# Performance work log

Hardware: AMD Instinct MI355X
Metric: run time of the kernel (lower is better)

## Reference

```python
import jax, jax.numpy as jnp
import numpy as np

DIM = 192; HEADS = 6; WS = 8; OVERLAP = 2; PAD = 3; STRIDE = WS - OVERLAP; HID = DIM * 4

_coords = np.stack(np.meshgrid(np.arange(WS), np.arange(WS), indexing='ij'), 0).reshape(2, -1)
_rel = (_coords[:, :, None] - _coords[:, None, :]).transpose(1, 2, 0).astype(np.int64)
_rel[..., 0] += WS - 1; _rel[..., 1] += WS - 1; _rel[..., 0] *= 2 * WS - 1
REL_IDX = jnp.asarray(_rel.sum(-1).reshape(-1))  # (WS^2 * WS^2,)


def _ln_c(x, g, b):
    # LayerNorm over channel dim of NCHW (LayerNormProxy)
    mu = jnp.mean(x, axis=1, keepdims=True)
    var = jnp.mean((x - mu) ** 2, axis=1, keepdims=True)
    return (x - mu) * jax.lax.rsqrt(var + 1e-5) * g[:, None, None] + b[:, None, None]


def _conv1x1(x, w, b):
    return jnp.einsum('bchw,oc->bohw', x, w) + b[:, None, None]


def _dwconv3(x, w, b):
    y = jax.lax.conv_general_dilated(x, w, (1, 1), ((1, 1), (1, 1)),
                                     feature_group_count=x.shape[1],
                                     dimension_numbers=('NCHW', 'OIHW', 'NCHW'))
    return y + b[:, None, None]


def _unfold(x, k, s, p):
    # F.unfold: (B,C,H,W) -> (B, C*k*k, L) with (C,kh,kw) channel order, row-major windows
    B, C, H, W = x.shape
    xp = jnp.pad(x, ((0, 0), (0, 0), (p, p), (p, p)))
    Lh = (H + 2 * p - k) // s + 1; Lw = (W + 2 * p - k) // s + 1
    ih = (jnp.arange(Lh) * s)[:, None] + jnp.arange(k)  # (Lh,k)
    iw = (jnp.arange(Lw) * s)[:, None] + jnp.arange(k)  # (Lw,k)
    t = xp[:, :, ih, :][:, :, :, :, iw]                 # (B,C,Lh,k,Lw,k)
    t = t.transpose(0, 1, 3, 5, 2, 4)                   # (B,C,k,k,Lh,Lw)
    return t.reshape(B, C * k * k, Lh * Lw)


def _fold(cols, h, w, k, s, p):
    # F.fold: (B, C*k*k, L) -> (B,C,h,w), summing overlaps
    B = cols.shape[0]
    Lh = (h + 2 * p - k) // s + 1; Lw = (w + 2 * p - k) // s + 1
    C = cols.shape[1] // (k * k)
    t = cols.reshape(B, C, k, k, Lh, Lw).transpose(0, 1, 4, 2, 5, 3)  # (B,C,Lh,k,Lw,k)
    ih = (jnp.arange(Lh) * s)[:, None] + jnp.arange(k)
    iw = (jnp.arange(Lw) * s)[:, None] + jnp.arange(k)
    out = jnp.zeros((B, C, h + 2 * p, w + 2 * p), cols.dtype)
    out = out.at[:, :, ih[:, :, None, None], iw[None, None, :, :]].add(t)
    return out[:, :, p:p + h, p:p + w]


def _reverse(win, h, w):
    B, L, nH, ws2, ch = win.shape
    cols = win.transpose(0, 2, 4, 3, 1).reshape(B, nH * ch * ws2, L)
    return _fold(cols, h, w, WS, STRIDE, PAD)


def _hft(x, w, b):
    # HFTAttention: high-frequency residual of multi-scale avg pools, dw-conv sigmoid gate
    B, C, h, ww = x.shape
    a = 3.0 * x
    for s in (2, 4, 8):
        pool = x.reshape(B, C, h // s, s, ww // s, s).mean(axis=(3, 5))
        a = a - jnp.repeat(jnp.repeat(pool, s, axis=2), s, axis=3)
    return jax.nn.sigmoid(_dwconv3(a, w, b)) * x


def _forward(x, n1g, n1b, qkv_w, qkv_b, temp, rpb, proj_w, proj_b, hft_w, hft_b,
             n2g, n2b, fc1_w, fc1_b, sgn_g, sgn_b, sg_w, sg_b, fc2_w, fc2_b):
    B, C, H, W = x.shape
    ch = C // HEADS
    y = _conv1x1(_ln_c(x, n1g, n1b), qkv_w, qkv_b)       # (B,3C,H,W)
    cols = _unfold(y, WS, STRIDE, PAD)
    L = cols.shape[-1]
    win = cols.reshape(B, 3 * HEADS, ch, WS * WS, L).transpose(0, 4, 1, 3, 2)  # (B,L,3H,ws2,ch)
    q = win[:, :, :HEADS] * temp[None, None]
    k = win[:, :, HEADS:2 * HEADS]
    v = win[:, :, 2 * HEADS:]
    attn = jnp.einsum('blhic,blhjc->blhij', q, k)
    bias = rpb[REL_IDX].reshape(WS * WS, WS * WS, HEADS).transpose(2, 0, 1)
    attn = attn + bias[None, None]
    e = jnp.exp(attn - jnp.max(attn, axis=-1, keepdims=True))
    s = jnp.sum(e, axis=-1, keepdims=True)               # (B,L,H,ws2,1)
    s_img = _reverse(s, H, W)                            # (B,HEADS,H,W): folded softmax denom
    o = jnp.einsum('blhij,blhjc->blhic', e, v)
    o_img = _reverse(o, H, W).reshape(B, HEADS, ch, H, W)
    out = (o_img / s_img[:, :, None]).reshape(B, C, H, W)
    out = _hft(_conv1x1(out, proj_w, proj_b), hft_w, hft_b)
    x1 = x + out
    z = jax.nn.gelu(_conv1x1(_ln_c(x1, n2g, n2b), fc1_w, fc1_b), approximate=False)
    z1, z2 = jnp.split(z, 2, axis=1)
    z = z1 * _dwconv3(_ln_c(z2, sgn_g, sgn_b), sg_w, sg_b)
    return x1 + _conv1x1(z, fc2_w, fc2_b)


def setup_inputs() -> dict:
    key = jax.random.key(0)
    ks = jax.random.split(key, 8)
    B, Hi, Wi = 4, 128, 128
    f = jnp.float32
    return {
        'x': jax.random.normal(ks[0], (B, DIM, Hi, Wi), f),
        'n1g': jnp.ones((DIM,), f), 'n1b': jnp.zeros((DIM,), f),
        'qkv_w': jax.random.normal(ks[1], (3 * DIM, DIM), f) * 0.02,
        'qkv_b': jnp.zeros((3 * DIM,), f),
        'temp': jnp.ones((HEADS, 1, 1), f),
        'rpb': jax.random.normal(ks[2], ((2 * WS - 1) ** 2, HEADS), f) * 0.02,
        'proj_w': jax.random.normal(ks[3], (DIM, DIM), f) * 0.02,
        'proj_b': jnp.zeros((DIM,), f),
        'hft_w': jax.random.normal(ks[4], (DIM, 1, 3, 3), f) * 0.02,
        'hft_b': jnp.zeros((DIM,), f),
        'n2g': jnp.ones((DIM,), f), 'n2b': jnp.zeros((DIM,), f),
        'fc1_w': jax.random.normal(ks[5], (HID, DIM), f) * 0.02,
        'fc1_b': jnp.zeros((HID,), f),
        'sgn_g': jnp.ones((HID // 2,), f), 'sgn_b': jnp.zeros((HID // 2,), f),
        'sg_w': jax.random.normal(ks[6], (HID // 2, 1, 3, 3), f) * 0.02,
        'sg_b': jnp.zeros((HID // 2,), f),
        'fc2_w': jax.random.normal(ks[7], (DIM, HID // 2), f) * 0.02,
        'fc2_b': jnp.zeros((DIM,), f),
    }


def reference(x, n1g, n1b, qkv_w, qkv_b, temp, rpb, proj_w, proj_b, hft_w, hft_b,
              n2g, n2b, fc1_w, fc1_b, sgn_g, sgn_b, sg_w, sg_b, fc2_w, fc2_b):
    return _forward(x, n1g, n1b, qkv_w, qkv_b, temp, rpb, proj_w, proj_b, hft_w, hft_b,
                    n2g, n2b, fc1_w, fc1_b, sgn_g, sgn_b, sg_w, sg_b, fc2_w, fc2_b)
```

## Files before the change

### kernel.cpp

```cpp
#include <hip/hip_runtime.h>
#include <math.h>

static constexpr int B_    = 4;
static constexpr int C_    = 192;
static constexpr int NPIX  = 16384;
static constexpr int PTOT  = B_ * NPIX;
static constexpr int HEADS = 6;
static constexpr int STR   = 6;
static constexpr int LH    = 22;
static constexpr int LWIN  = LH * LH;
static constexpr int NWIN  = B_ * LWIN;

typedef short bf16x8 __attribute__((ext_vector_type(8)));
typedef float f32x4  __attribute__((ext_vector_type(4)));

__device__ __forceinline__ unsigned short f2bf(float f) {
    union { float f; unsigned int u; } v; v.f = f;
    return (unsigned short)((v.u + 0x8000u) >> 16);
}
__device__ __forceinline__ float bf2f(unsigned short h) {
    union { unsigned int u; float f; } v; v.u = ((unsigned int)h) << 16;
    return v.f;
}
__device__ __forceinline__ unsigned int pack2bf(float a, float b) {
    union { float f; unsigned int u; } x, y; x.f = a; y.f = b;
    return __builtin_amdgcn_perm(y.u + 0x8000u, x.u + 0x8000u, 0x07060302u);
}
__device__ __forceinline__ float gelu_f(float v) {
    float vv = v * v;
    float u  = v * fmaf(vv, 0.0713548162f, 1.5957691216f);
    float ue = (u > 80.f) ? 80.f : u;
    float e  = __expf(ue);
    float r  = __builtin_amdgcn_rcpf(e + 1.f);
    return v * e * r;
}

__global__ __launch_bounds__(256) void prep_k(const float* __restrict__ W, const float* __restrict__ g,
                                              const float* __restrict__ bln, const float* __restrict__ bias,
                                              int M, int K,
                                              unsigned short* __restrict__ wgb, float* __restrict__ wsum,
                                              float* __restrict__ wb) {
    int o = blockIdx.x * 256 + threadIdx.x;
    if (o >= M) return;
    float sum = 0.f, bb = 0.f;
    for (int c = 0; c < K; ++c) {
        float wv = W[(size_t)o * K + c];
        float wgv = wv * g[c];
        wgb[(size_t)o * K + c] = f2bf(wgv);
        sum += wgv;
        bb += wv * bln[c];
    }
    wsum[o] = sum;
    wb[o] = bb + bias[o];
}

__global__ __launch_bounds__(256) void wcvt_k(const float* __restrict__ W, unsigned short* __restrict__ Wb, int n) {
    int i = blockIdx.x * 256 + threadIdx.x;
    if (i < n) Wb[i] = f2bf(W[i]);
}

template <typename T, bool LNS>
__global__ __launch_bounds__(256) void transpose_k(const T* __restrict__ in, unsigned short* __restrict__ out,
                                                   int Cn, int bstride, float2* __restrict__ ps) {
    __shared__ float tile[64][65];
    int n0 = blockIdx.x << 6, c0 = blockIdx.y << 6, b = blockIdx.z;
    int t = threadIdx.x, r = t >> 2, cg = (t & 3) << 4;
    const T* ib = in + (size_t)b * bstride;
    if constexpr (sizeof(T) == 4) {
        const float4* src = (const float4*)(ib + (size_t)(c0 + r) * NPIX + n0 + cg);
        #pragma unroll
        for (int j = 0; j < 4; ++j) {
            float4 v = src[j];
            tile[r][cg + 4 * j + 0] = v.x; tile[r][cg + 4 * j + 1] = v.y;
            tile[r][cg + 4 * j + 2] = v.z; tile[r][cg + 4 * j + 3] = v.w;
        }
    } else {
        const uint4* src = (const uint4*)((const unsigned short*)ib + (size_t)(c0 + r) * NPIX + n0 + cg);
        uint4 v0 = src[0], v1 = src[1];
        unsigned int arr[8] = {v0.x, v0.y, v0.z, v0.w, v1.x, v1.y, v1.z, v1.w};
        #pragma unroll
        for (int j = 0; j < 8; ++j) {
            tile[r][cg + 2 * j]     = bf2f((unsigned short)(arr[j] & 0xFFFFu));
            tile[r][cg + 2 * j + 1] = bf2f((unsigned short)(arr[j] >> 16));
        }
    }
    __syncthreads();
    unsigned int pk[8];
    float s = 0.f, s2 = 0.f;
    #pragma unroll
    for (int j = 0; j < 8; ++j) {
        float a  = tile[cg + 2 * j][r];
        float c2 = tile[cg + 2 * j + 1][r];
        if (LNS) { s += a + c2; s2 += a * a + c2 * c2; }
        pk[j] = pack2bf(a, c2);
    }
    uint4* dst = (uint4*)(out + ((size_t)(b << 14) + n0 + r) * Cn + c0 + cg);
    dst[0] = make_uint4(pk[0], pk[1], pk[2], pk[3]);
    dst[1] = make_uint4(pk[4], pk[5], pk[6], pk[7]);
    if (LNS) {
        s  += __shfl_xor(s, 1);  s  += __shfl_xor(s, 2);
        s2 += __shfl_xor(s2, 1); s2 += __shfl_xor(s2, 2);
        if ((t & 3) == 0)
            ps[((b * gridDim.y + blockIdx.y) << 14) + n0 + r] = make_float2(s, s2);
    }
}

__global__ __launch_bounds__(256) void lnfin_k(const float2* __restrict__ ps, int nch, float invC,
                                               float* __restrict__ mu, float* __restrict__ rs) {
    int p = blockIdx.x * 256 + threadIdx.x;
    int b = p >> 14, n = p & (NPIX - 1);
    float s = 0.f, s2 = 0.f;
    for (int c = 0; c < nch; ++c) {
        float2 v = ps[((b * nch + c) << 14) + n];
        s += v.x; s2 += v.y;
    }
    float m = s * invC;
    mu[p] = m;
    rs[p] = rsqrtf(s2 * invC - m * m + 1e-5f);
}

__global__ __launch_bounds__(256) void lnstats_z2_k(const unsigned short* __restrict__ z,
                                                    float* __restrict__ mu, float* __restrict__ rs) {
    __shared__ float red[2][4][64];
    int n0 = blockIdx.x << 6, b = blockIdx.y;
    int t = threadIdx.x;
    int px = n0 + (t & 63), cg = t >> 6;
    float s = 0.f, s2 = 0.f;
    for (int c = cg; c < 384; c += 4) {
        float v = bf2f(z[((size_t)(b * 768 + 384 + c) << 14) + px]);
        s += v; s2 += v * v;
    }
    red[0][cg][t & 63] = s;
    red[1][cg][t & 63] = s2;
    __syncthreads();
    if (t < 64) {
        float ss  = red[0][0][t] + red[0][1][t] + red[0][2][t] + red[0][3][t];
        float ss2 = red[1][0][t] + red[1][1][t] + red[1][2][t] + red[1][3][t];
        float m = ss * (1.f / 384.f);
        mu[(b << 14) + n0 + t] = m;
        rs[(b << 14) + n0 + t] = rsqrtf(ss2 * (1.f / 384.f) - m * m + 1e-5f);
    }
}

template <int KK, int MPB, int ACT, bool LN, bool RES, bool OBF>
__global__ __launch_bounds__(256) void gemm2_k(const unsigned short* __restrict__ Wb,
                                               const unsigned short* __restrict__ Xt,
                                               void* __restrict__ outv,
                                               const float* __restrict__ mu, const float* __restrict__ rs,
                                               const float* __restrict__ wsum, const float* __restrict__ wb,
                                               const float* __restrict__ resid, int M) {
    constexpr int LDK    = KK + 8;
    constexpr int KSTEPS = KK / 32;
    constexpr int PFG    = (KSTEPS > 6) ? 6 : KSTEPS;
    __shared__ unsigned short xs[64 * LDK];

    int t = threadIdx.x;
    int pt = blockIdx.x;
    int b  = pt >> 8;
    int n0 = (pt & 255) << 6;

    const unsigned short* xg = Xt + (size_t)(b * NPIX + n0) * KK;
    constexpr int NJ = KK / 8;
    #pragma unroll
    for (int i = 0; i < 64 * NJ / 256; ++i) {
        int c = i * 256 + t;
        int p, j;
        if (KK == 192) { p = (c * 2731) >> 16; j = c - p * 24; }
        else           { int q = c >> 4; p = (q * 21846) >> 16; j = c - p * 48; }
        uint4 v = *(const uint4*)(xg + (size_t)c * 8);
        *(uint4*)&xs[p * LDK + j * 8] = v;
    }
    __syncthreads();

    int w  = t >> 6, l = t & 63;
    int wr = w >> 1, wc = w & 1;
    int lr = l & 15, kb = l >> 4;
    int pw = wr * 32;

    bf16x8 afr[KSTEPS][2];
    #pragma unroll
    for (int ks = 0; ks < KSTEPS; ++ks)
        #pragma unroll
        for (int m = 0; m < 2; ++m)
            afr[ks][m] = *(const bf16x8*)&xs[(pw + m * 16 + lr) * LDK + ks * 32 + kb * 8];

    float rsv[2][4], murs[2][4];
    if (LN) {
        #pragma unroll
        for (int m = 0; m < 2; ++m) {
            int nidx = n0 + pw + m * 16 + kb * 4;
            #pragma unroll
            for (int r = 0; r < 4; ++r) {
                float mv = mu[(b << 14) + nidx + r];
                rsv[m][r] = rs[(b << 14) + nidx + r];
                murs[m][r] = mv * rsv[m][r];
            }
        }
    }

    int ocbase = blockIdx.y * MPB;
    #pragma unroll
    for (int oc = 0; oc < MPB; ++oc) {
        int ow = ((ocbase + oc) << 6) + wc * 32;
        f32x4 acc[2][2];
        #pragma unroll
        for (int m = 0; m < 2; ++m)
            #pragma unroll
            for (int n = 0; n < 2; ++n) acc[m][n] = (f32x4){0.f, 0.f, 0.f, 0.f};

        #pragma unroll
        for (int kg = 0; kg < KSTEPS; kg += PFG) {
            bf16x8 bfr[PFG][2];
            #pragma unroll
            for (int kk = 0; kk < PFG; ++kk)
                #pragma unroll
                for (int n = 0; n < 2; ++n)
                    bfr[kk][n] = *(const bf16x8*)(Wb + (size_t)(ow + n * 16 + lr) * KK + (kg + kk) * 32 + kb * 8);
            #pragma unroll
            for (int kk = 0; kk < PFG; ++kk)
                #pragma unroll
                for (int m = 0; m < 2; ++m)
                    #pragma unroll
                    for (int n = 0; n < 2; ++n)
                        acc[m][n] = __builtin_amdgcn_mfma_f32_16x16x32_bf16(afr[kg + kk][m], bfr[kk][n], acc[m][n], 0, 0, 0);
        }

        #pragma unroll
        for (int m = 0; m < 2; ++m) {
            int nidx = n0 + pw + m * 16 + kb * 4;
            #pragma unroll
            for (int n = 0; n < 2; ++n) {
                int o = ow + n * 16 + lr;
                float wbv = wb[o];
                float wsv = 0.f; if (LN) wsv = wsum[o];
                size_t obase = (((size_t)b * M + o) << 14) + nidx;
                float rv[4] = {0.f, 0.f, 0.f, 0.f};
                if (RES) {
                    float4 rr = *(const float4*)(resid + obase);
                    rv[0] = rr.x; rv[1] = rr.y; rv[2] = rr.z; rv[3] = rr.w;
                }
                float vo[4];
                #pragma unroll
                for (int r = 0; r < 4; ++r) {
                    float a = acc[m][n][r];
                    float v;
                    if (LN) { float t1 = fmaf(-murs[m][r], wsv, wbv); v = fmaf(rsv[m][r], a, t1); }
                    else    v = a + wbv;
                    if (ACT == 1) v = gelu_f(v);
                    vo[r] = v + rv[r];
                }
                if (OBF) {
                    uint2 u;
                    u.x = pack2bf(vo[0], vo[1]);
                    u.y = pack2bf(vo[2], vo[3]);
                    *(uint2*)((unsigned short*)outv + obase) = u;
                } else {
                    float4 f = {vo[0], vo[1], vo[2], vo[3]};
                    *(float4*)((float*)outv + obase) = f;
                }
            }
        }
    }
}

__global__ __launch_bounds__(64) void attn_mfma_k(const unsigned short* __restrict__ qkv,
                                                  const float* __restrict__ rpb,
                                                  const float* __restrict__ temp,
                                                  unsigned short* __restrict__ o_win,
                                                  float* __restrict__ s_win) {
    __shared__ unsigned short p_lds[64 * 72];
    __shared__ float rp[225];
    int wh = blockIdx.x;
    int head = wh % HEADS;
    int bw = wh / HEADS;
    int b = bw / LWIN, l = bw % LWIN;
    int sh = l / LH, sw = l % LH;
    int h0 = sh * STR - 3, w0 = sw * STR - 3;
    int t = threadIdx.x;
    int lr = t & 15, kb = t >> 4;

    for (int i = t; i < 225; i += 64) rp[i] = rpb[i * HEADS + head];
    float tmp = temp[head];

    const size_t qbase = ((size_t)(b * 576 + head * 32)) << 14;
    const unsigned short* qp = qkv + qbase;
    const unsigned short* kp = qkv + qbase + ((size_t)192 << 14);
    const unsigned short* vp = qkv + qbase + ((size_t)384 << 14);

    bf16x8 kf[4], qf[4];
    #pragma unroll
    for (int m = 0; m < 4; ++m) {
        int jp = m * 16 + lr;
        int hh = h0 + (jp >> 3), ww = w0 + (jp & 7);
        bool ok = ((unsigned)hh < 128u) && ((unsigned)ww < 128u);
        int pix = (hh << 7) + ww;
        #pragma unroll
        for (int j = 0; j < 8; ++j) {
            unsigned short kv = 0, qv = 0;
            if (ok) {
                size_t off = ((size_t)(kb * 8 + j) << 14) + pix;
                kv = kp[off];
                qv = qp[off];
            }
            kf[m][j] = (short)kv;
            qf[m][j] = (short)qv;
        }
    }

    f32x4 st[4][4];
    #pragma unroll
    for (int m = 0; m < 4; ++m)
        #pragma unroll
        for (int n = 0; n < 4; ++n) st[m][n] = (f32x4){0.f, 0.f, 0.f, 0.f};
    #pragma unroll
    for (int m = 0; m < 4; ++m)
        #pragma unroll
        for (int n = 0; n < 4; ++n)
            st[m][n] = __builtin_amdgcn_mfma_f32_16x16x32_bf16(kf[m], qf[n], st[m][n], 0, 0, 0);

    bf16x8 vf[2][2];
    #pragma unroll
    for (int np = 0; np < 2; ++np) {
        #pragma unroll
        for (int ks = 0; ks < 2; ++ks) {
            int hh = h0 + ks * 4 + kb;
            bool okr = (unsigned)hh < 128u;
            const unsigned short* vrow = vp + (((size_t)(np * 16 + lr)) << 14) + (hh << 7) + w0;
            #pragma unroll
            for (int j = 0; j < 8; ++j) {
                int ww = w0 + j;
                unsigned short vv = 0;
                if (okr && (unsigned)ww < 128u) vv = vrow[j];
                vf[np][ks][j] = (short)vv;
            }
        }
    }

    __syncthreads();

    #pragma unroll
    for (int n = 0; n < 4; ++n) {
        int i = n * 16 + lr;
        int iyy = i >> 3, ixx = i & 7;
        #pragma unroll
        for (int m = 0; m < 4; ++m) {
            #pragma unroll
            for (int r = 0; r < 4; ++r) {
                int j = m * 16 + kb * 4 + r;
                int dy = iyy - (j >> 3) + 7;
                int dx = ixx - (j & 7) + 7;
                st[m][n][r] = st[m][n][r] * tmp + rp[dy * 15 + dx];
            }
        }
    }

    #pragma unroll
    for (int n = 0; n < 4; ++n) {
        float mx = -1e30f;
        #pragma unroll
        for (int m = 0; m < 4; ++m)
            #pragma unroll
            for (int r = 0; r < 4; ++r) mx = fmaxf(mx, st[m][n][r]);
        mx = fmaxf(mx, __shfl_xor(mx, 16));
        mx = fmaxf(mx, __shfl_xor(mx, 32));
        float s = 0.f;
        #pragma unroll
        for (int m = 0; m < 4; ++m) {
            #pragma unroll
            for (int r = 0; r < 4; ++r) {
                float e = __expf(st[m][n][r] - mx);
                st[m][n][r] = e;
                s += e;
            }
        }
        s += __shfl_xor(s, 16);
        s += __shfl_xor(s, 32);
        int i = n * 16 + lr;
        if (kb == 0) s_win[(size_t)wh * 64 + i] = s;
        #pragma unroll
        for (int m = 0; m < 4; ++m) {
            *(unsigned int*)&p_lds[i * 72 + m * 16 + kb * 4]     = pack2bf(st[m][n][0], st[m][n][1]);
            *(unsigned int*)&p_lds[i * 72 + m * 16 + kb * 4 + 2] = pack2bf(st[m][n][2], st[m][n][3]);
        }
    }

    __syncthreads();

    f32x4 oc[4][2];
    #pragma unroll
    for (int m = 0; m < 4; ++m)
        #pragma unroll
        for (int np = 0; np < 2; ++np) oc[m][np] = (f32x4){0.f, 0.f, 0.f, 0.f};
    #pragma unroll
    for (int ks = 0; ks < 2; ++ks) {
        bf16x8 pa[4];
        #pragma unroll
        for (int m = 0; m < 4; ++m)
            pa[m] = *(const bf16x8*)&p_lds[(m * 16 + lr) * 72 + ks * 32 + kb * 8];
        #pragma unroll
        for (int m = 0; m < 4; ++m)
            #pragma unroll
            for (int np = 0; np < 2; ++np)
                oc[m][np] = __builtin_amdgcn_mfma_f32_16x16x32_bf16(pa[m], vf[np][ks], oc[m][np], 0, 0, 0);
    }

    unsigned short* ob = o_win + (size_t)wh * 2048;
    #pragma unroll
    for (int m = 0; m < 4; ++m) {
        int ibase = m * 16 + kb * 4;
        #pragma unroll
        for (int np = 0; np < 2; ++np) {
            int c = np * 16 + lr;
            #pragma unroll
            for (int r = 0; r < 4; ++r)
                ob[(ibase + r) * 32 + c] = f2bf(oc[m][np][r]);
        }
    }
}

__device__ __forceinline__ void win_range(int h, int& s0, int& s1) {
    s0 = (h + 1) / 6; if (s0 < 0) s0 = 0;
    s1 = (h + 3) / 6; if (s1 > 21) s1 = 21;
}

__global__ __launch_bounds__(256) void simg_k(const float* __restrict__ s_win, float* __restrict__ s_img) {
    int tid = blockIdx.x * 256 + threadIdx.x;
    if (tid >= B_ * HEADS * NPIX) return;
    int n = tid & (NPIX - 1);
    int bh = tid >> 14;
    int hd = bh % HEADS, b = bh / HEADS;
    int hy = n >> 7, wx = n & 127;
    int sy0, sy1, sx0, sx1;
    win_range(hy, sy0, sy1);
    win_range(wx, sx0, sx1);
    float acc = 0.f;
    for (int sy = sy0; sy <= sy1; ++sy)
        for (int sx = sx0; sx <= sx1; ++sx) {
            int idx = (hy - (sy * 6 - 3)) * 8 + (wx - (sx * 6 - 3));
            acc += s_win[(size_t)((b * LWIN + sy * LH + sx) * HEADS + hd) * 64 + idx];
        }
    s_img[tid] = acc;
}

__global__ __launch_bounds__(256) void fold_k(const unsigned short* __restrict__ o_win,
                                              const float* __restrict__ s_img,
                                              unsigned short* __restrict__ attn_t) {
    int tid = blockIdx.x * 256 + threadIdx.x;
    int q = (int)((((unsigned long long)(tid >> 3)) * 174763ull) >> 19);
    int oct = tid - q * 24;
    int n = q & (NPIX - 1), b = q >> 14;
    int hd = oct >> 2, c8 = (oct & 3) << 3;
    int hy = n >> 7, wx = n & 127;
    int sy0, sy1, sx0, sx1;
    win_range(hy, sy0, sy1);
    win_range(wx, sx0, sx1);
    float acc[8] = {0.f, 0.f, 0.f, 0.f, 0.f, 0.f, 0.f, 0.f};
    for (int sy = sy0; sy <= sy1; ++sy)
        for (int sx = sx0; sx <= sx1; ++sx) {
            int idx = (hy - (sy * 6 - 3)) * 8 + (wx - (sx * 6 - 3));
            const unsigned short* p = o_win + ((size_t)((b * LWIN + sy * LH + sx) * HEADS + hd) * 2048 + idx * 32 + c8);
            uint4 v = *(const uint4*)p;
            unsigned int arr[4] = {v.x, v.y, v.z, v.w};
            #pragma unroll
            for (int j = 0; j < 4; ++j) {
                acc[2 * j]     += bf2f((unsigned short)(arr[j] & 0xFFFFu));
                acc[2 * j + 1] += bf2f((unsigned short)(arr[j] >> 16));
            }
        }
    float inv = __builtin_amdgcn_rcpf(s_img[((b * HEADS + hd) << 14) + n]);
    unsigned int pk[4];
    #pragma unroll
    for (int j = 0; j < 4; ++j)
        pk[j] = pack2bf(acc[2 * j] * inv, acc[2 * j + 1] * inv);
    *(uint4*)&attn_t[((size_t)((b << 14) + n)) * 192 + hd * 32 + c8] = make_uint4(pk[0], pk[1], pk[2], pk[3]);
}

template <typename TI>
__global__ __launch_bounds__(256) void halve_k(const TI* __restrict__ in, float* __restrict__ out, int Win) {
    int Wo = Win >> 1;
    int tot = B_ * C_ * Wo * Wo;
    int tid = blockIdx.x * 256 + threadIdx.x;
    if (tid >= tot) return;
    int xy = tid % (Wo * Wo);
    int bc = tid / (Wo * Wo);
    int y = xy / Wo, x = xy % Wo;
    const TI* p = in + (size_t)bc * Win * Win + (size_t)(2 * y) * Win + 2 * x;
    float a, bq, c, d;
    if constexpr (sizeof(TI) == 2) {
        a = bf2f(p[0]); bq = bf2f(p[1]); c = bf2f(p[Win]); d = bf2f(p[Win + 1]);
    } else {
        a = p[0]; bq = p[1]; c = p[Win]; d = p[Win + 1];
    }
    out[tid] = 0.25f * (a + bq + c + d);
}

__global__ __launch_bounds__(256) void hft_fused_k(const unsigned short* __restrict__ po, const float* __restrict__ x,
                                                   const float* __restrict__ p2, const float* __restrict__ p4,
                                                   const float* __restrict__ p8, const float* __restrict__ hw,
                                                   const float* __restrict__ hb, float* __restrict__ x1) {
    __shared__ float tile[34 * 133];
    int rt = blockIdx.x, ch = blockIdx.y, b = blockIdx.z;
    int bc = b * C_ + ch;
    int y0 = rt << 5;
    int t = threadIdx.x;
    const unsigned short* pob = po + ((size_t)bc << 14);
    const float* p2b = p2 + ((size_t)bc << 12);
    const float* p4b = p4 + ((size_t)bc << 10);
    const float* p8b = p8 + ((size_t)bc << 8);

    for (int idx = t; idx < 34 * 133; idx += 256) {
        int row = idx / 133, col = idx - row * 133;
        int yy = y0 + row - 1, xw = col - 1;
        float val = 0.f;
        if (col < 130 && (unsigned)yy < 128u && (unsigned)xw < 128u) {
            int nn = (yy << 7) + xw;
            val = 3.f * bf2f(pob[nn])
                - p2b[((yy >> 1) << 6) + (xw >> 1)]
                - p4b[((yy >> 2) << 5) + (xw >> 2)]
                - p8b[((yy >> 3) << 4) + (xw >> 3)];
        }
        tile[idx] = val;
    }
    __syncthreads();

    float wv[9];
    #pragma unroll
    for (int k = 0; k < 9; ++k) wv[k] = hw[ch * 9 + k];
    float hbv = hb[ch];

    int r = t & 31, c0 = (t >> 5) << 4;
    int nbase = ((y0 + r) << 7) + c0;
    const float* xb = x + ((size_t)bc << 14);
    float* x1b = x1 + ((size_t)bc << 14);

    float pov[16], xv[16];
    {
        const uint4* pp4 = (const uint4*)(pob + nbase);
        uint4 a0 = pp4[0], a1 = pp4[1];
        unsigned int arr[8] = {a0.x, a0.y, a0.z, a0.w, a1.x, a1.y, a1.z, a1.w};
        #pragma unroll
        for (int j = 0; j < 8; ++j) {
            pov[2 * j]     = bf2f((unsigned short)(arr[j] & 0xFFFFu));
            pov[2 * j + 1] = bf2f((unsigned short)(arr[j] >> 16));
        }
        #pragma unroll
        for (int j4 = 0; j4 < 4; ++j4) {
            float4 xx = *(const float4*)(xb + nbase + 4 * j4);
            xv[4*j4] = xx.x; xv[4*j4+1] = xx.y; xv[4*j4+2] = xx.z; xv[4*j4+3] = xx.w;
        }
    }
    float res[16];
    #pragma unroll
    for (int j = 0; j < 16; ++j) {
        float acc = hbv;
        #pragma unroll
        for (int dy = 0; dy < 3; ++dy)
            #pragma unroll
            for (int dx = 0; dx < 3; ++dx)
                acc += wv[dy * 3 + dx] * tile[(r + dy) * 133 + c0 + j + dx];
        float sg = __builtin_amdgcn_rcpf(1.f + __expf(-acc));
        res[j] = xv[j] + sg * pov[j];
    }
    #pragma unroll
    for (int j4 = 0; j4 < 4; ++j4) {
        float4 o = {res[4*j4], res[4*j4+1], res[4*j4+2], res[4*j4+3]};
        *(float4*)(x1b + nbase + 4 * j4) = o;
    }
}

__global__ __launch_bounds__(256) void sgmul_k(unsigned short* __restrict__ z,
                                               const float* __restrict__ mu3, const float* __restrict__ rs3,
                                               const float* __restrict__ sgn_g, const float* __restrict__ sgn_b,
                                               const float* __restrict__ sg_w, const float* __restrict__ sg_b) {
    __shared__ float tile[34 * 133];
    int rt = blockIdx.x, ch = blockIdx.y, b = blockIdx.z;
    int y0 = rt << 5;
    int t = threadIdx.x;
    const unsigned short* zb = z + ((size_t)(b * 768 + 384 + ch) << 14);
    unsigned short* z1p = z + ((size_t)(b * 768 + ch) << 14);
    const float* mub = mu3 + (b << 14);
    const float* rsb = rs3 + (b << 14);
    float g = sgn_g[ch], bb = sgn_b[ch];

    for (int idx = t; idx < 34 * 133; idx += 256) {
        int row = idx / 133, col = idx - row * 133;
        int yy = y0 + row - 1, xw = col - 1;
        float val = 0.f;
        if (col < 130 && (unsigned)yy < 128u && (unsigned)xw < 128u) {
            int nn = (yy << 7) + xw;
            val = (bf2f(zb[nn]) - mub[nn]) * rsb[nn] * g + bb;
        }
        tile[idx] = val;
    }
    __syncthreads();

    float wv[9];
    #pragma unroll
    for (int k = 0; k < 9; ++k) wv[k] = sg_w[ch * 9 + k];
    float sb = sg_b[ch];

    int r = t & 31, c0 = (t >> 5) << 4;
    int nbase = ((y0 + r) << 7) + c0;

    float res[16];
    #pragma unroll
    for (int j = 0; j < 16; ++j) {
        float acc = sb;
        #pragma unroll
        for (int dy = 0; dy < 3; ++dy)
            #pragma unroll
            for (int dx = 0; dx < 3; ++dx)
                acc += wv[dy * 3 + dx] * tile[(r + dy) * 133 + c0 + j + dx];
        res[j] = acc;
    }
    uint4* zp = (uint4*)(z1p + nbase);
    uint4 v0 = zp[0], v1 = zp[1];
    unsigned int arr[8] = {v0.x, v0.y, v0.z, v0.w, v1.x, v1.y, v1.z, v1.w};
    #pragma unroll
    for (int j = 0; j < 8; ++j) {
        float lo = bf2f((unsigned short)(arr[j] & 0xFFFFu)) * res[2 * j];
        float hi = bf2f((unsigned short)(arr[j] >> 16)) * res[2 * j + 1];
        arr[j] = pack2bf(lo, hi);
    }
    zp[0] = make_uint4(arr[0], arr[1], arr[2], arr[3]);
    zp[1] = make_uint4(arr[4], arr[5], arr[6], arr[7]);
}

extern "C" void kernel_launch(void* const* d_in, const int* in_sizes, int n_in,
                              void* d_out, int out_size, void* d_ws, size_t ws_size,
                              hipStream_t stream) {
    const float* x     = (const float*)d_in[0];
    const float* n1g   = (const float*)d_in[1];
    const float* n1b   = (const float*)d_in[2];
    const float* qkv_w = (const float*)d_in[3];
    const float* qkv_b = (const float*)d_in[4];
    const float* temp  = (const float*)d_in[5];
    const float* rpb   = (const float*)d_in[6];
    const float* proj_w= (const float*)d_in[7];
    const float* proj_b= (const float*)d_in[8];
    const float* hft_w = (const float*)d_in[9];
    const float* hft_b = (const float*)d_in[10];
    const float* n2g   = (const float*)d_in[11];
    const float* n2b   = (const float*)d_in[12];
    const float* fc1_w = (const float*)d_in[13];
    const float* fc1_b = (const float*)d_in[14];
    const float* sgn_g = (const float*)d_in[15];
    const float* sgn_b = (const float*)d_in[16];
    const float* sg_w  = (const float*)d_in[17];
    const float* sg_b  = (const float*)d_in[18];
    const float* fc2_w = (const float*)d_in[19];
    const float* fc2_b = (const float*)d_in[20];
    float* out = (float*)d_out;
    float* w = (float*)d_ws;

    float* mu1 = w;            float* rs1 = w + 65536;
    float* mu2 = w + 131072;   float* rs2 = w + 196608;
    float* mu3 = w + 262144;   float* rs3 = w + 327680;
    unsigned short* wgb_qkv = (unsigned short*)(w + 393216);
    float* wsum_qkv = w + 448512;  float* wb_qkv = w + 449088;
    unsigned short* wgb_fc1 = (unsigned short*)(w + 449664);
    float* wsum_fc1 = w + 523392;  float* wb_fc1 = w + 524160;
    unsigned short* pwb  = (unsigned short*)(w + 524928);
    unsigned short* f2wb = (unsigned short*)(w + 543360);
    unsigned short* xt     = (unsigned short*)(w + 580224);
    unsigned short* attn_t = xt;
    unsigned short* qkvb = (unsigned short*)(w + 6871680);
    unsigned short* proj_out = (unsigned short*)(w + 6871680);
    float* p2 = w + 19454592;  float* p4 = w + 22600320;  float* p8 = w + 23386752;
    unsigned short* x1t  = (unsigned short*)(w + 6871680);
    unsigned short* z1t  = (unsigned short*)(w + 6871680);
    unsigned short* o_win = (unsigned short*)(w + 25746048);
    float* s_win = w + 49535616;
    float* s_img = w + 50279040;
    unsigned short* z = (unsigned short*)(w + 25746048);
    float* x1 = w + 50911872;
    float2* ps = (float2*)(w + 19454592);

    transpose_k<float, true><<<dim3(256, 3, B_), 256, 0, stream>>>(x, xt, 192, 192 * NPIX, ps);
    lnfin_k<<<256, 256, 0, stream>>>(ps, 3, 1.f / 192.f, mu1, rs1);
    prep_k<<<3, 256, 0, stream>>>(qkv_w, n1g, n1b, qkv_b, 576, 192, wgb_qkv, wsum_qkv, wb_qkv);
    gemm2_k<192, 3, 0, true, false, true><<<dim3(1024, 3), 256, 0, stream>>>(
        wgb_qkv, xt, qkvb, mu1, rs1, wsum_qkv, wb_qkv, nullptr, 576);
    attn_mfma_k<<<NWIN * HEADS, 64, 0, stream>>>(qkvb, rpb, temp, o_win, s_win);
    simg_k<<<1536, 256, 0, stream>>>(s_win, s_img);
    fold_k<<<6144, 256, 0, stream>>>(o_win, s_img, attn_t);
    wcvt_k<<<144, 256, 0, stream>>>(proj_w, pwb, 192 * 192);
    gemm2_k<192, 1, 0, false, false, true><<<dim3(1024, 3), 256, 0, stream>>>(
        pwb, attn_t, proj_out, nullptr, nullptr, nullptr, proj_b, nullptr, 192);
    halve_k<unsigned short><<<12288, 256, 0, stream>>>(proj_out, p2, 128);
    halve_k<float><<<3072, 256, 0, stream>>>(p2, p4, 64);
    halve_k<float><<<768, 256, 0, stream>>>(p4, p8, 32);
    hft_fused_k<<<dim3(4, 192, B_), 256, 0, stream>>>(proj_out, x, p2, p4, p8, hft_w, hft_b, x1);
    transpose_k<float, true><<<dim3(256, 3, B_), 256, 0, stream>>>(x1, x1t, 192, 192 * NPIX, ps);
    lnfin_k<<<256, 256, 0, stream>>>(ps, 3, 1.f / 192.f, mu2, rs2);
    prep_k<<<3, 256, 0, stream>>>(fc1_w, n2g, n2b, fc1_b, 768, 192, wgb_fc1, wsum_fc1, wb_fc1);
    gemm2_k<192, 6, 1, true, false, true><<<dim3(1024, 2), 256, 0, stream>>>(
        wgb_fc1, x1t, z, mu2, rs2, wsum_fc1, wb_fc1, nullptr, 768);
    lnstats_z2_k<<<dim3(256, B_), 256, 0, stream>>>(z, mu3, rs3);
    sgmul_k<<<dim3(4, 384, B_), 256, 0, stream>>>(z, mu3, rs3, sgn_g, sgn_b, sg_w, sg_b);
    transpose_k<unsigned short, false><<<dim3(256, 6, B_), 256, 0, stream>>>(z, z1t, 384, 768 * NPIX, nullptr);
    wcvt_k<<<288, 256, 0, stream>>>(fc2_w, f2wb, 192 * 384);
    gemm2_k<384, 3, 0, false, true, false><<<dim3(1024, 1), 256, 0, stream>>>(
        f2wb, z1t, out, nullptr, nullptr, nullptr, fc2_b, x1, 192);
}
```

Before: 666.7 us.

## Halve GEMM pixel tile and let each block cover all output channels

The pointwise GEMM kernel now stages 32 pixels per block instead of 64, and each block loops over every output-channel tile (grid y collapsed to 1, 2048 blocks). That cuts the per-wave A-fragment registers and LDS footprint, and it removes the repeated staging of the same pixel tile across grid-y blocks. In exchange the weights are streamed from global/L2 more times per pixel, each wave does half the MFMAs per weight load, and the oc loop is only partially unrolled.

```diff
diff --git a/kernel.cpp b/kernel.cpp
--- a/kernel.cpp
+++ b/kernel.cpp
@@ -143,7 +143,7 @@
 }
 
 template <int KK, int MPB, int ACT, bool LN, bool RES, bool OBF>
-__global__ __launch_bounds__(256) void gemm2_k(const unsigned short* __restrict__ Wb,
+__global__ __launch_bounds__(256) void gemm3_k(const unsigned short* __restrict__ Wb,
                                                const unsigned short* __restrict__ Xt,
                                                void* __restrict__ outv,
                                                const float* __restrict__ mu, const float* __restrict__ rs,
@@ -151,22 +151,22 @@
                                                const float* __restrict__ resid, int M) {
     constexpr int LDK    = KK + 8;
     constexpr int KSTEPS = KK / 32;
-    constexpr int PFG    = (KSTEPS > 6) ? 6 : KSTEPS;
-    __shared__ unsigned short xs[64 * LDK];
+    constexpr int PFG    = 3;
+    __shared__ unsigned short xs[32 * LDK];
 
     int t = threadIdx.x;
     int pt = blockIdx.x;
-    int b  = pt >> 8;
-    int n0 = (pt & 255) << 6;
+    int b  = pt >> 9;
+    int n0 = (pt & 511) << 5;
 
     const unsigned short* xg = Xt + (size_t)(b * NPIX + n0) * KK;
-    constexpr int NJ = KK / 8;
-    #pragma unroll
-    for (int i = 0; i < 64 * NJ / 256; ++i) {
+    constexpr int NCH = 32 * KK / 8;
+    #pragma unroll
+    for (int i = 0; i < NCH / 256; ++i) {
         int c = i * 256 + t;
         int p, j;
         if (KK == 192) { p = (c * 2731) >> 16; j = c - p * 24; }
-        else           { int q = c >> 4; p = (q * 21846) >> 16; j = c - p * 48; }
+        else           { p = (c * 21846) >> 20; j = c - p * 48; }
         uint4 v = *(const uint4*)(xg + (size_t)c * 8);
         *(uint4*)&xs[p * LDK + j * 8] = v;
     }
@@ -175,38 +175,31 @@
     int w  = t >> 6, l = t & 63;
     int wr = w >> 1, wc = w & 1;
     int lr = l & 15, kb = l >> 4;
-    int pw = wr * 32;
-
-    bf16x8 afr[KSTEPS][2];
+    int pw = wr * 16;
+
+    bf16x8 afr[KSTEPS];
     #pragma unroll
     for (int ks = 0; ks < KSTEPS; ++ks)
-        #pragma unroll
-        for (int m = 0; m < 2; ++m)
-            afr[ks][m] = *(const bf16x8*)&xs[(pw + m * 16 + lr) * LDK + ks * 32 + kb * 8];
-
-    float rsv[2][4], murs[2][4];
+        afr[ks] = *(const bf16x8*)&xs[(pw + lr) * LDK + ks * 32 + kb * 8];
+
+    float rsv[4], murs[4];
     if (LN) {
-        #pragma unroll
-        for (int m = 0; m < 2; ++m) {
-            int nidx = n0 + pw + m * 16 + kb * 4;
-            #pragma unroll
-            for (int r = 0; r < 4; ++r) {
-                float mv = mu[(b << 14) + nidx + r];
-                rsv[m][r] = rs[(b << 14) + nidx + r];
-                murs[m][r] = mv * rsv[m][r];
-            }
+        int nidx = n0 + pw + kb * 4;
+        #pragma unroll
+        for (int r = 0; r < 4; ++r) {
+            float mv = mu[(b << 14) + nidx + r];
+            rsv[r] = rs[(b << 14) + nidx + r];
+            murs[r] = mv * rsv[r];
         }
     }
 
     int ocbase = blockIdx.y * MPB;
-    #pragma unroll
+    #pragma unroll 2
     for (int oc = 0; oc < MPB; ++oc) {
         int ow = ((ocbase + oc) << 6) + wc * 32;
-        f32x4 acc[2][2];
-        #pragma unroll
-        for (int m = 0; m < 2; ++m)
-            #pragma unroll
-            for (int n = 0; n < 2; ++n) acc[m][n] = (f32x4){0.f, 0.f, 0.f, 0.f};
+        f32x4 acc[2];
+        acc[0] = (f32x4){0.f, 0.f, 0.f, 0.f};
+        acc[1] = (f32x4){0.f, 0.f, 0.f, 0.f};
 
         #pragma unroll
         for (int kg = 0; kg < KSTEPS; kg += PFG) {
@@ -219,45 +212,40 @@
             #pragma unroll
             for (int kk = 0; kk < PFG; ++kk)
                 #pragma unroll
-                for (int m = 0; m < 2; ++m)
-                    #pragma unroll
-                    for (int n = 0; n < 2; ++n)
-                        acc[m][n] = __builtin_amdgcn_mfma_f32_16x16x32_bf16(afr[kg + kk][m], bfr[kk][n], acc[m][n], 0, 0, 0);
-        }
-
-        #pragma unroll
-        for (int m = 0; m < 2; ++m) {
-            int nidx = n0 + pw + m * 16 + kb * 4;
-            #pragma unroll
-            for (int n = 0; n < 2; ++n) {
-                int o = ow + n * 16 + lr;
-                float wbv = wb[o];
-                float wsv = 0.f; if (LN) wsv = wsum[o];
-                size_t obase = (((size_t)b * M + o) << 14) + nidx;
-                float rv[4] = {0.f, 0.f, 0.f, 0.f};
-                if (RES) {
-                    float4 rr = *(const float4*)(resid + obase);
-                    rv[0] = rr.x; rv[1] = rr.y; rv[2] = rr.z; rv[3] = rr.w;
-                }
-                float vo[4];
-                #pragma unroll
-                for (int r = 0; r < 4; ++r) {
-                    float a = acc[m][n][r];
-                    float v;
-                    if (LN) { float t1 = fmaf(-murs[m][r], wsv, wbv); v = fmaf(rsv[m][r], a, t1); }
-                    else    v = a + wbv;
-                    if (ACT == 1) v = gelu_f(v);
-                    vo[r] = v + rv[r];
-                }
-                if (OBF) {
-                    uint2 u;
-                    u.x = pack2bf(vo[0], vo[1]);
-                    u.y = pack2bf(vo[2], vo[3]);
-                    *(uint2*)((unsigned short*)outv + obase) = u;
-                } else {
-                    float4 f = {vo[0], vo[1], vo[2], vo[3]};
-                    *(float4*)((float*)outv + obase) = f;
-                }
+                for (int n = 0; n < 2; ++n)
+                    acc[n] = __builtin_amdgcn_mfma_f32_16x16x32_bf16(afr[kg + kk], bfr[kk][n], acc[n], 0, 0, 0);
+        }
+
+        int nidx = n0 + pw + kb * 4;
+        #pragma unroll
+        for (int n = 0; n < 2; ++n) {
+            int o = ow + n * 16 + lr;
+            float wbv = wb[o];
+            float wsv = 0.f; if (LN) wsv = wsum[o];
+            size_t obase = (((size_t)b * M + o) << 14) + nidx;
+            float rv[4] = {0.f, 0.f, 0.f, 0.f};
+            if (RES) {
+                float4 rr = *(const float4*)(resid + obase);
+                rv[0] = rr.x; rv[1] = rr.y; rv[2] = rr.z; rv[3] = rr.w;
+            }
+            float vo[4];
+            #pragma unroll
+            for (int r = 0; r < 4; ++r) {
+                float a = acc[n][r];
+                float v;
+                if (LN) { float t1 = fmaf(-murs[r], wsv, wbv); v = fmaf(rsv[r], a, t1); }
+                else    v = a + wbv;
+                if (ACT == 1) v = gelu_f(v);
+                vo[r] = v + rv[r];
+            }
+            if (OBF) {
+                uint2 u;
+                u.x = pack2bf(vo[0], vo[1]);
+                u.y = pack2bf(vo[2], vo[3]);
+                *(uint2*)((unsigned short*)outv + obase) = u;
+            } else {
+                float4 f = {vo[0], vo[1], vo[2], vo[3]};
+                *(float4*)((float*)outv + obase) = f;
             }
         }
     }
@@ -679,13 +667,13 @@
     transpose_k<float, true><<<dim3(256, 3, B_), 256, 0, stream>>>(x, xt, 192, 192 * NPIX, ps);
     lnfin_k<<<256, 256, 0, stream>>>(ps, 3, 1.f / 192.f, mu1, rs1);
     prep_k<<<3, 256, 0, stream>>>(qkv_w, n1g, n1b, qkv_b, 576, 192, wgb_qkv, wsum_qkv, wb_qkv);
-    gemm2_k<192, 3, 0, true, false, true><<<dim3(1024, 3), 256, 0, stream>>>(
+    gemm3_k<192, 9, 0, true, false, true><<<dim3(2048, 1), 256, 0, stream>>>(
         wgb_qkv, xt, qkvb, mu1, rs1, wsum_qkv, wb_qkv, nullptr, 576);
     attn_mfma_k<<<NWIN * HEADS, 64, 0, stream>>>(qkvb, rpb, temp, o_win, s_win);
     simg_k<<<1536, 256, 0, stream>>>(s_win, s_img);
     fold_k<<<6144, 256, 0, stream>>>(o_win, s_img, attn_t);
     wcvt_k<<<144, 256, 0, stream>>>(proj_w, pwb, 192 * 192);
-    gemm2_k<192, 1, 0, false, false, true><<<dim3(1024, 3), 256, 0, stream>>>(
+    gemm3_k<192, 3, 0, false, false, true><<<dim3(2048, 1), 256, 0, stream>>>(
         pwb, attn_t, proj_out, nullptr, nullptr, nullptr, proj_b, nullptr, 192);
     halve_k<unsigned short><<<12288, 256, 0, stream>>>(proj_out, p2, 128);
     halve_k<float><<<3072, 256, 0, stream>>>(p2, p4, 64);
@@ -694,12 +682,12 @@
     transpose_k<float, true><<<dim3(256, 3, B_), 256, 0, stream>>>(x1, x1t, 192, 192 * NPIX, ps);
     lnfin_k<<<256, 256, 0, stream>>>(ps, 3, 1.f / 192.f, mu2, rs2);
     prep_k<<<3, 256, 0, stream>>>(fc1_w, n2g, n2b, fc1_b, 768, 192, wgb_fc1, wsum_fc1, wb_fc1);
-    gemm2_k<192, 6, 1, true, false, true><<<dim3(1024, 2), 256, 0, stream>>>(
+    gemm3_k<192, 12, 1, true, false, true><<<dim3(2048, 1), 256, 0, stream>>>(
         wgb_fc1, x1t, z, mu2, rs2, wsum_fc1, wb_fc1, nullptr, 768);
     lnstats_z2_k<<<dim3(256, B_), 256, 0, stream>>>(z, mu3, rs3);
     sgmul_k<<<dim3(4, 384, B_), 256, 0, stream>>>(z, mu3, rs3, sgn_g, sgn_b, sg_w, sg_b);
     transpose_k<unsigned short, false><<<dim3(256, 6, B_), 256, 0, stream>>>(z, z1t, 384, 768 * NPIX, nullptr);
     wcvt_k<<<288, 256, 0, stream>>>(fc2_w, f2wb, 192 * 384);
-    gemm2_k<384, 3, 0, false, true, false><<<dim3(1024, 1), 256, 0, stream>>>(
+    gemm3_k<384, 3, 0, false, true, false><<<dim3(2048, 1), 256, 0, stream>>>(
         f2wb, z1t, out, nullptr, nullptr, nullptr, fc2_b, x1, 192);
 }
```

Result: slower. 800.1 us (+20.0%).

## Fuse NCHW transpose and LayerNorm stats into GEMM input staging

Applied to the files above, without the earlier changes.

Removes the separate transpose and LN-statistics kernels. The GEMM now loads NCHW activations directly (fp32 or bf16), transposes them into shared memory, and computes per-pixel mean and rstd in-block. The QKV and fc1 GEMMs now run one block per pixel tile covering all output channels (MPB 9/12), so the input is staged once instead of being reloaded per column group. This cuts the global round-trips of transposed copies, but the staging loads are scalar strided reads and the shared-memory writes are 2-byte, which may bank-conflict. The blocks are also longer and there are fewer of them.

```diff
diff --git a/kernel.cpp b/kernel.cpp
--- a/kernel.cpp
+++ b/kernel.cpp
@@ -59,66 +59,6 @@
     if (i < n) Wb[i] = f2bf(W[i]);
 }
 
-template <typename T, bool LNS>
-__global__ __launch_bounds__(256) void transpose_k(const T* __restrict__ in, unsigned short* __restrict__ out,
-                                                   int Cn, int bstride, float2* __restrict__ ps) {
-    __shared__ float tile[64][65];
-    int n0 = blockIdx.x << 6, c0 = blockIdx.y << 6, b = blockIdx.z;
-    int t = threadIdx.x, r = t >> 2, cg = (t & 3) << 4;
-    const T* ib = in + (size_t)b * bstride;
-    if constexpr (sizeof(T) == 4) {
-        const float4* src = (const float4*)(ib + (size_t)(c0 + r) * NPIX + n0 + cg);
-        #pragma unroll
-        for (int j = 0; j < 4; ++j) {
-            float4 v = src[j];
-            tile[r][cg + 4 * j + 0] = v.x; tile[r][cg + 4 * j + 1] = v.y;
-            tile[r][cg + 4 * j + 2] = v.z; tile[r][cg + 4 * j + 3] = v.w;
-        }
-    } else {
-        const uint4* src = (const uint4*)((const unsigned short*)ib + (size_t)(c0 + r) * NPIX + n0 + cg);
-        uint4 v0 = src[0], v1 = src[1];
-        unsigned int arr[8] = {v0.x, v0.y, v0.z, v0.w, v1.x, v1.y, v1.z, v1.w};
-        #pragma unroll
-        for (int j = 0; j < 8; ++j) {
-            tile[r][cg + 2 * j]     = bf2f((unsigned short)(arr[j] & 0xFFFFu));
-            tile[r][cg + 2 * j + 1] = bf2f((unsigned short)(arr[j] >> 16));
-        }
-    }
-    __syncthreads();
-    unsigned int pk[8];
-    float s = 0.f, s2 = 0.f;
-    #pragma unroll
-    for (int j = 0; j < 8; ++j) {
-        float a  = tile[cg + 2 * j][r];
-        float c2 = tile[cg + 2 * j + 1][r];
-        if (LNS) { s += a + c2; s2 += a * a + c2 * c2; }
-        pk[j] = pack2bf(a, c2);
-    }
-    uint4* dst = (uint4*)(out + ((size_t)(b << 14) + n0 + r) * Cn + c0 + cg);
-    dst[0] = make_uint4(pk[0], pk[1], pk[2], pk[3]);
-    dst[1] = make_uint4(pk[4], pk[5], pk[6], pk[7]);
-    if (LNS) {
-        s  += __shfl_xor(s, 1);  s  += __shfl_xor(s, 2);
-        s2 += __shfl_xor(s2, 1); s2 += __shfl_xor(s2, 2);
-        if ((t & 3) == 0)
-            ps[((b * gridDim.y + blockIdx.y) << 14) + n0 + r] = make_float2(s, s2);
-    }
-}
-
-__global__ __launch_bounds__(256) void lnfin_k(const float2* __restrict__ ps, int nch, float invC,
-                                               float* __restrict__ mu, float* __restrict__ rs) {
-    int p = blockIdx.x * 256 + threadIdx.x;
-    int b = p >> 14, n = p & (NPIX - 1);
-    float s = 0.f, s2 = 0.f;
-    for (int c = 0; c < nch; ++c) {
-        float2 v = ps[((b * nch + c) << 14) + n];
-        s += v.x; s2 += v.y;
-    }
-    float m = s * invC;
-    mu[p] = m;
-    rs[p] = rsqrtf(s2 * invC - m * m + 1e-5f);
-}
-
 __global__ __launch_bounds__(256) void lnstats_z2_k(const unsigned short* __restrict__ z,
                                                     float* __restrict__ mu, float* __restrict__ rs) {
     __shared__ float red[2][4][64];
@@ -142,33 +82,67 @@
     }
 }
 
-template <int KK, int MPB, int ACT, bool LN, bool RES, bool OBF>
-__global__ __launch_bounds__(256) void gemm2_k(const unsigned short* __restrict__ Wb,
-                                               const unsigned short* __restrict__ Xt,
+template <int KK, int INMODE, int MPB, int ACT, bool LN, bool RES, bool OBF>
+__global__ __launch_bounds__(256) void gemm4_k(const unsigned short* __restrict__ Wb,
+                                               const void* __restrict__ Xin,
                                                void* __restrict__ outv,
-                                               const float* __restrict__ mu, const float* __restrict__ rs,
                                                const float* __restrict__ wsum, const float* __restrict__ wb,
-                                               const float* __restrict__ resid, int M) {
-    constexpr int LDK    = KK + 8;
-    constexpr int KSTEPS = KK / 32;
-    constexpr int PFG    = (KSTEPS > 6) ? 6 : KSTEPS;
+                                               const float* __restrict__ resid, int M, int bstride) {
+    constexpr int LDK     = KK + 8;
+    constexpr int KSTEPS  = KK / 32;
+    constexpr int PFG     = (KSTEPS > 6) ? 6 : KSTEPS;
     __shared__ unsigned short xs[64 * LDK];
+    __shared__ float sred[2][4][64];
+    __shared__ float muL[64], rsL[64];
 
     int t = threadIdx.x;
     int pt = blockIdx.x;
     int b  = pt >> 8;
     int n0 = (pt & 255) << 6;
 
-    const unsigned short* xg = Xt + (size_t)(b * NPIX + n0) * KK;
-    constexpr int NJ = KK / 8;
-    #pragma unroll
-    for (int i = 0; i < 64 * NJ / 256; ++i) {
-        int c = i * 256 + t;
-        int p, j;
-        if (KK == 192) { p = (c * 2731) >> 16; j = c - p * 24; }
-        else           { int q = c >> 4; p = (q * 21846) >> 16; j = c - p * 48; }
-        uint4 v = *(const uint4*)(xg + (size_t)c * 8);
-        *(uint4*)&xs[p * LDK + j * 8] = v;
+    if constexpr (INMODE == 0) {
+        const unsigned short* xg = (const unsigned short*)Xin + (size_t)(b * NPIX + n0) * KK;
+        constexpr int NJ = KK / 8;
+        #pragma unroll
+        for (int i = 0; i < 64 * NJ / 256; ++i) {
+            int c = i * 256 + t;
+            int p, j;
+            if (KK == 192) { p = (c * 2731) >> 16; j = c - p * 24; }
+            else           { int q = c >> 4; p = (q * 21846) >> 16; j = c - p * 48; }
+            uint4 v = *(const uint4*)(xg + (size_t)c * 8);
+            *(uint4*)&xs[p * LDK + j * 8] = v;
+        }
+    } else if constexpr (INMODE == 1) {
+        const float* xg = (const float*)Xin + (size_t)b * bstride + n0;
+        int px = t & 63, c0 = t >> 6;
+        float s = 0.f, s2 = 0.f;
+        #pragma unroll 4
+        for (int st = 0; st < KK / 4; ++st) {
+            int c = c0 + 4 * st;
+            float v = xg[(size_t)c * NPIX + px];
+            s += v; s2 += v * v;
+            xs[px * LDK + c] = f2bf(v);
+        }
+        sred[0][c0][px] = s;
+        sred[1][c0][px] = s2;
+        __syncthreads();
+        if (t < 64) {
+            float ss  = sred[0][0][t] + sred[0][1][t] + sred[0][2][t] + sred[0][3][t];
+            float ss2 = sred[1][0][t] + sred[1][1][t] + sred[1][2][t] + sred[1][3][t];
+            float m = ss * (1.f / (float)KK);
+            muL[t] = m;
+            rsL[t] = rsqrtf(ss2 * (1.f / (float)KK) - m * m + 1e-5f);
+        }
+    } else {
+        const unsigned short* xg = (const unsigned short*)Xin + (size_t)b * bstride + n0;
+        int px2 = (t & 31) << 1, c0 = t >> 5;
+        #pragma unroll 4
+        for (int st = 0; st < KK / 8; ++st) {
+            int c = c0 + 8 * st;
+            unsigned int v = *(const unsigned int*)(xg + (size_t)c * NPIX + px2);
+            xs[px2 * LDK + c]       = (unsigned short)(v & 0xFFFFu);
+            xs[(px2 + 1) * LDK + c] = (unsigned short)(v >> 16);
+        }
     }
     __syncthreads();
 
@@ -188,18 +162,18 @@
     if (LN) {
         #pragma unroll
         for (int m = 0; m < 2; ++m) {
-            int nidx = n0 + pw + m * 16 + kb * 4;
+            int pl = pw + m * 16 + kb * 4;
             #pragma unroll
             for (int r = 0; r < 4; ++r) {
-                float mv = mu[(b << 14) + nidx + r];
-                rsv[m][r] = rs[(b << 14) + nidx + r];
+                float mv = muL[pl + r];
+                rsv[m][r] = rsL[pl + r];
                 murs[m][r] = mv * rsv[m][r];
             }
         }
     }
 
     int ocbase = blockIdx.y * MPB;
-    #pragma unroll
+    #pragma unroll 2
     for (int oc = 0; oc < MPB; ++oc) {
         int ow = ((ocbase + oc) << 6) + wc * 32;
         f32x4 acc[2][2];
@@ -653,8 +627,6 @@
     float* out = (float*)d_out;
     float* w = (float*)d_ws;
 
-    float* mu1 = w;            float* rs1 = w + 65536;
-    float* mu2 = w + 131072;   float* rs2 = w + 196608;
     float* mu3 = w + 262144;   float* rs3 = w + 327680;
     unsigned short* wgb_qkv = (unsigned short*)(w + 393216);
     float* wsum_qkv = w + 448512;  float* wb_qkv = w + 449088;
@@ -662,44 +634,35 @@
     float* wsum_fc1 = w + 523392;  float* wb_fc1 = w + 524160;
     unsigned short* pwb  = (unsigned short*)(w + 524928);
     unsigned short* f2wb = (unsigned short*)(w + 543360);
-    unsigned short* xt     = (unsigned short*)(w + 580224);
-    unsigned short* attn_t = xt;
+    unsigned short* attn_t = (unsigned short*)(w + 580224);
     unsigned short* qkvb = (unsigned short*)(w + 6871680);
     unsigned short* proj_out = (unsigned short*)(w + 6871680);
     float* p2 = w + 19454592;  float* p4 = w + 22600320;  float* p8 = w + 23386752;
-    unsigned short* x1t  = (unsigned short*)(w + 6871680);
-    unsigned short* z1t  = (unsigned short*)(w + 6871680);
     unsigned short* o_win = (unsigned short*)(w + 25746048);
     float* s_win = w + 49535616;
     float* s_img = w + 50279040;
     unsigned short* z = (unsigned short*)(w + 25746048);
     float* x1 = w + 50911872;
-    float2* ps = (float2*)(w + 19454592);
-
-    transpose_k<float, true><<<dim3(256, 3, B_), 256, 0, stream>>>(x, xt, 192, 192 * NPIX, ps);
-    lnfin_k<<<256, 256, 0, stream>>>(ps, 3, 1.f / 192.f, mu1, rs1);
+
     prep_k<<<3, 256, 0, stream>>>(qkv_w, n1g, n1b, qkv_b, 576, 192, wgb_qkv, wsum_qkv, wb_qkv);
-    gemm2_k<192, 3, 0, true, false, true><<<dim3(1024, 3), 256, 0, stream>>>(
-        wgb_qkv, xt, qkvb, mu1, rs1, wsum_qkv, wb_qkv, nullptr, 576);
+    gemm4_k<192, 1, 9, 0, true, false, true><<<dim3(1024, 1), 256, 0, stream>>>(
+        wgb_qkv, x, qkvb, wsum_qkv, wb_qkv, nullptr, 576, 192 * NPIX);
     attn_mfma_k<<<NWIN * HEADS, 64, 0, stream>>>(qkvb, rpb, temp, o_win, s_win);
     simg_k<<<1536, 256, 0, stream>>>(s_win, s_img);
     fold_k<<<6144, 256, 0, stream>>>(o_win, s_img, attn_t);
     wcvt_k<<<144, 256, 0, stream>>>(proj_w, pwb, 192 * 192);
-    gemm2_k<192, 1, 0, false, false, true><<<dim3(1024, 3), 256, 0, stream>>>(
-        pwb, attn_t, proj_out, nullptr, nullptr, nullptr, proj_b, nullptr, 192);
+    gemm4_k<192, 0, 1, 0, false, false, true><<<dim3(1024, 3), 256, 0, stream>>>(
+        pwb, attn_t, proj_out, nullptr, proj_b, nullptr, 192, 0);
     halve_k<unsigned short><<<12288, 256, 0, stream>>>(proj_out, p2, 128);
     halve_k<float><<<3072, 256, 0, stream>>>(p2, p4, 64);
     halve_k<float><<<768, 256, 0, stream>>>(p4, p8, 32);
     hft_fused_k<<<dim3(4, 192, B_), 256, 0, stream>>>(proj_out, x, p2, p4, p8, hft_w, hft_b, x1);
-    transpose_k<float, true><<<dim3(256, 3, B_), 256, 0, stream>>>(x1, x1t, 192, 192 * NPIX, ps);
-    lnfin_k<<<256, 256, 0, stream>>>(ps, 3, 1.f / 192.f, mu2, rs2);
     prep_k<<<3, 256, 0, stream>>>(fc1_w, n2g, n2b, fc1_b, 768, 192, wgb_fc1, wsum_fc1, wb_fc1);
-    gemm2_k<192, 6, 1, true, false, true><<<dim3(1024, 2), 256, 0, stream>>>(
-        wgb_fc1, x1t, z, mu2, rs2, wsum_fc1, wb_fc1, nullptr, 768);
+    gemm4_k<192, 1, 12, 1, true, false, true><<<dim3(1024, 1), 256, 0, stream>>>(
+        wgb_fc1, x1, z, wsum_fc1, wb_fc1, nullptr, 768, 192 * NPIX);
     lnstats_z2_k<<<dim3(256, B_), 256, 0, stream>>>(z, mu3, rs3);
     sgmul_k<<<dim3(4, 384, B_), 256, 0, stream>>>(z, mu3, rs3, sgn_g, sgn_b, sg_w, sg_b);
-    transpose_k<unsigned short, false><<<dim3(256, 6, B_), 256, 0, stream>>>(z, z1t, 384, 768 * NPIX, nullptr);
     wcvt_k<<<288, 256, 0, stream>>>(fc2_w, f2wb, 192 * 384);
-    gemm2_k<384, 3, 0, false, true, false><<<dim3(1024, 1), 256, 0, stream>>>(
-        f2wb, z1t, out, nullptr, nullptr, nullptr, fc2_b, x1, 192);
-}
+    gemm4_k<384, 2, 3, 0, false, true, false><<<dim3(1024, 1), 256, 0, stream>>>(
+        f2wb, z, out, nullptr, fc2_b, x1, 192, 768 * NPIX);
+}
```

After: 628.8 us. 5.7% less time.
